# Kernel optimization log

Measured on AMD Instinct MI355X. Metric: run time of the kernel, lower is better.

Reference implementation:

```python
import jax, jax.numpy as jnp
import numpy as np

L = 3          # encoder layers
H, D = 12, 64  # heads, head_dim
DM = H * D     # 768
DF = 3072
WH = WW = 14
S = WH * WW + 1            # 197 tokens incl. cls
ND = (2*WH-1)*(2*WW-1) + 3  # 732 rel-pos entries
EPS = 1e-12


def _make_rel_idx():
    coords = np.stack(np.meshgrid(np.arange(WH), np.arange(WW), indexing='ij'))
    coords = coords.reshape(2, -1)                      # [2, 196]
    rel = (coords[:, :, None] - coords[:, None, :]).transpose(1, 2, 0)  # [196,196,2]
    rel[:, :, 0] += WH - 1
    rel[:, :, 1] += WW - 1
    rel[:, :, 0] *= 2 * WW - 1
    idx = np.zeros((S, S), dtype=np.int32)
    idx[1:, 1:] = rel.sum(-1)
    idx[0, :] = ND - 3
    idx[:, 0] = ND - 2
    idx[0, 0] = ND - 1
    return jnp.asarray(idx.flatten())

REL_IDX = _make_rel_idx()


def _ln(x, g, b):
    m = jnp.mean(x, -1, keepdims=True)
    v = jnp.mean(jnp.square(x - m), -1, keepdims=True)
    return (x - m) * jax.lax.rsqrt(v + EPS) * g + b


def setup_inputs() -> dict:
    key = jax.random.key(0)
    ks = iter(jax.random.split(key, 32))
    p = lambda *s: jax.random.normal(next(ks), s, jnp.float32) * 0.02
    inp = {
        'x': jax.random.normal(next(ks), (64, WH, WW, DM), jnp.float32),
        'cls': p(1, 1, DM),
        'g1': jnp.ones((L, DM)), 'b1': jnp.zeros((L, DM)),
        'Wq': p(L, DM, DM), 'bq': jnp.zeros((L, DM)),
        'Wk': p(L, DM, DM),
        'Wv': p(L, DM, DM), 'bv': jnp.zeros((L, DM)),
        'rel_tbl': p(L, ND, H),
        'Wo': p(L, DM, DM), 'bo': jnp.zeros((L, DM)),
        'lam1': jnp.full((L, DM), 0.1),
        'g2': jnp.ones((L, DM)), 'b2': jnp.zeros((L, DM)),
        'Wi': p(L, DM, DF), 'bi': jnp.zeros((L, DF)),
        'Wmo': p(L, DF, DM), 'bmo': jnp.zeros((L, DM)),
        'lam2': jnp.full((L, DM), 0.1),
    }
    return inp


def reference(x, cls, g1, b1, Wq, bq, Wk, Wv, bv, rel_tbl, Wo, bo, lam1,
              g2, b2, Wi, bi, Wmo, bmo, lam2):
    B = x.shape[0]
    # patchemb: NHWC -> NCHW -> [B, C, HW] -> [B, HW, C], prepend cls token
    t = jnp.transpose(x, (0, 3, 1, 2)).reshape(B, DM, WH * WW)
    t = jnp.transpose(t, (0, 2, 1))
    h = jnp.concatenate([jnp.broadcast_to(cls, (B, 1, DM)), t], axis=1)  # [B,S,DM]

    scale = 1.0 / np.sqrt(D)
    for i in range(L):
        r = h
        hn = _ln(h, g1[i], b1[i])
        q = (hn @ Wq[i] + bq[i]).reshape(B, S, H, D)
        k = (hn @ Wk[i]).reshape(B, S, H, D)
        v = (hn @ Wv[i] + bv[i]).reshape(B, S, H, D)
        scores = jnp.einsum('bqhd,bkhd->bhqk', q, k) * scale   # [B,H,S,S]
        rel = rel_tbl[i][REL_IDX].reshape(S, S, H)             # gather bias table
        scores = scores + jnp.transpose(rel, (2, 0, 1))[None]
        probs = jax.nn.softmax(scores, axis=-1)
        ctx = jnp.einsum('bhqk,bkhd->bqhd', probs, v).reshape(B, S, DM)
        h = r + (ctx @ Wo[i] + bo[i]) * lam1[i]
        r = h
        hn = _ln(h, g2[i], b2[i])
        ff = jax.nn.gelu(hn @ Wi[i] + bi[i], approximate=False) @ Wmo[i] + bmo[i]
        h = r + ff * lam2[i]
    return h  # final encoder output [B, S, DM]
```

## Files before the change

kernel.cpp:

```cpp
#include <hip/hip_runtime.h>

#define DMM 768
#define DFF 3072
#define NH  12
#define HD  64
#define SQ  197
#define BA  64
#define NDD 732
#define MROWS (BA*SQ)
#define MPAD  12672
#define PCOLS 224
#define KS2   72
#define VTS   232
#define QS    2304

typedef unsigned short u16;
typedef __bf16 bf16x8 __attribute__((ext_vector_type(8)));
typedef float  f32x4  __attribute__((ext_vector_type(4)));
typedef unsigned short us8 __attribute__((ext_vector_type(8)));

__device__ __forceinline__ float b2f(u16 u) {
    unsigned v = ((unsigned)u) << 16;
    float f; __builtin_memcpy(&f, &v, 4); return f;
}
__device__ __forceinline__ u16 f2b(float f) {
    unsigned v; __builtin_memcpy(&v, &f, 4);
    unsigned r = v + 0x7FFFu + ((v >> 16) & 1u);
    return (u16)(r >> 16);
}
__device__ __forceinline__ float gelu_exact(float x) {
    return 0.5f * x * (1.0f + erff(x * 0.70710678118654752f));
}
__device__ __forceinline__ void gload16(const u16* g, u16* l) {
    __builtin_amdgcn_global_load_lds(
        (const __attribute__((address_space(1))) unsigned int*)(g),
        (__attribute__((address_space(3))) unsigned int*)(l), 16, 0, 0);
}
__device__ __forceinline__ void hard_barrier() {
    asm volatile("s_waitcnt lgkmcnt(0)" ::: "memory");
    __builtin_amdgcn_s_barrier();
}

__global__ void patch_k(const float* __restrict__ x, const float* __restrict__ cls,
                        float* __restrict__ h) {
    long idx = (long)blockIdx.x * 256 + threadIdx.x;
    if (idx >= (long)MPAD * DMM) return;
    long r = idx / DMM; int c = (int)(idx % DMM);
    float v = 0.0f;
    if (r < MROWS) {
        int b = (int)(r / SQ), s = (int)(r % SQ);
        v = (s == 0) ? cls[c] : x[((long)b * 196 + (s - 1)) * DMM + c];
    }
    h[idx] = v;
}

__global__ void out_k(const float* __restrict__ h, float* __restrict__ out) {
    long idx = (long)blockIdx.x * 256 + threadIdx.x;
    if (idx < (long)MROWS * DMM) out[idx] = h[idx];
}

__global__ __launch_bounds__(256) void tcast_k(const float* __restrict__ in,
                                               u16* __restrict__ out,
                                               int Kd, int Nd) {
    __shared__ float t[32][33];
    int k0 = blockIdx.x * 32, n0 = blockIdx.y * 32;
    int tx = threadIdx.x & 31, ty = threadIdx.x >> 5;
    #pragma unroll
    for (int i = 0; i < 4; ++i)
        t[tx][ty + 8 * i] = in[(long)(k0 + ty + 8 * i) * Nd + n0 + tx];
    __syncthreads();
    #pragma unroll
    for (int i = 0; i < 4; ++i)
        out[(long)(n0 + ty + 8 * i) * Kd + k0 + tx] = f2b(t[ty + 8 * i][tx]);
}

__global__ __launch_bounds__(256) void ln_k(const float* __restrict__ h,
                                            const float* __restrict__ g,
                                            const float* __restrict__ b,
                                            u16* __restrict__ hn) {
    int row = blockIdx.x, tid = threadIdx.x;
    const float* hr = h + (long)row * DMM;
    float x0 = hr[tid], x1 = hr[tid + 256], x2 = hr[tid + 512];
    float s = x0 + x1 + x2, sq = x0 * x0 + x1 * x1 + x2 * x2;
    #pragma unroll
    for (int m = 32; m > 0; m >>= 1) {
        s  += __shfl_xor(s,  m, 64);
        sq += __shfl_xor(sq, m, 64);
    }
    __shared__ float ls[4], lq[4];
    int w = tid >> 6;
    if ((tid & 63) == 0) { ls[w] = s; lq[w] = sq; }
    __syncthreads();
    s  = ls[0] + ls[1] + ls[2] + ls[3];
    sq = lq[0] + lq[1] + lq[2] + lq[3];
    float mean = s * (1.0f / DMM);
    float var  = fmaxf(sq * (1.0f / DMM) - mean * mean, 0.0f);
    float rs = rsqrtf(var + 1e-12f);
    u16* hnr = hn + (long)row * DMM;
    hnr[tid]       = f2b((x0 - mean) * rs * g[tid]       + b[tid]);
    hnr[tid + 256] = f2b((x1 - mean) * rs * g[tid + 256] + b[tid + 256]);
    hnr[tid + 512] = f2b((x2 - mean) * rs * g[tid + 512] + b[tid + 512]);
}

__global__ void bqkv_k(const float* __restrict__ bq, const float* __restrict__ bv,
                       float* __restrict__ out) {
    int i = blockIdx.x * 256 + threadIdx.x;
    if (i >= QS) return;
    out[i] = (i < 768) ? bq[i] : ((i < 1536) ? 0.0f : bv[i - 1536]);
}

template <int EPI>
__global__ __launch_bounds__(256) void gemm_bt(
    const u16* __restrict__ A, const u16* __restrict__ BT,
    const float* __restrict__ bias, u16* __restrict__ outB,
    float* __restrict__ hio, const float* __restrict__ lam,
    int K, int N) {
    __shared__ __align__(16) u16 pool[16896];
    int tid = threadIdx.x;
    int w = tid >> 6, lane = tid & 63;
    int wr = w >> 1, wc = w & 1;
    int m16 = lane & 15;
    int kq  = (lane >> 4) * 8;
    int kq4 = (lane >> 4) * 4;

    int nwg = gridDim.x, bid = blockIdx.x;
    int qd = nwg >> 3, rm = nwg & 7;
    int xcd = bid & 7, seq = bid >> 3;
    int wg = (xcd < rm ? xcd * (qd + 1) : rm * (qd + 1) + (xcd - rm) * qd) + seq;
    int ntn = N >> 7;
    long m0 = (long)(wg / ntn) * 128;
    long n0 = (long)(wg % ntn) * 128;

    f32x4 acc[4][4] = {};

    int row_a = tid >> 2;
    int col_a = (tid & 3) * 8;
    const u16* gA0 = &A[(m0 + row_a) * (long)K + col_a];
    const u16* gA1 = &A[(m0 + 64 + row_a) * (long)K + col_a];
    const u16* gB0 = &BT[(n0 + row_a) * (long)K + col_a];
    const u16* gB1 = &BT[(n0 + 64 + row_a) * (long)K + col_a];
    int wo = w * 512;

    u16* const b0 = pool;
    u16* const b1 = pool + 8192;

    auto stage = [&](int k, u16* buf) {
        int k0 = k << 5;
        gload16(gA0 + k0, buf + wo);
        gload16(gA1 + k0, buf + 2048 + wo);
        gload16(gB0 + k0, buf + 4096 + wo);
        gload16(gB1 + k0, buf + 6144 + wo);
    };
    auto compute = [&](const u16* buf) {
        bf16x8 af[4], bf[4];
        #pragma unroll
        for (int i = 0; i < 4; ++i)
            af[i] = *(const bf16x8*)&buf[(wr * 64 + i * 16 + m16) * 32 + kq];
        #pragma unroll
        for (int j = 0; j < 4; ++j)
            bf[j] = *(const bf16x8*)&buf[4096 + (wc * 64 + j * 16 + m16) * 32 + kq];
        #pragma unroll
        for (int i = 0; i < 4; ++i)
            #pragma unroll
            for (int j = 0; j < 4; ++j)
                acc[i][j] = __builtin_amdgcn_mfma_f32_16x16x32_bf16(
                    af[i], bf[j], acc[i][j], 0, 0, 0);
    };

    const int nsteps = K >> 5;
    stage(0, b0);
    for (int ks = 0; ks < nsteps - 2; ks += 2) {
        stage(ks + 1, b1);
        asm volatile("s_waitcnt vmcnt(4)" ::: "memory");
        __builtin_amdgcn_s_barrier();
        compute(b0);
        hard_barrier();
        stage(ks + 2, b0);
        asm volatile("s_waitcnt vmcnt(4)" ::: "memory");
        __builtin_amdgcn_s_barrier();
        compute(b1);
        hard_barrier();
    }
    stage(nsteps - 1, b1);
    asm volatile("s_waitcnt vmcnt(4)" ::: "memory");
    __builtin_amdgcn_s_barrier();
    compute(b0);
    hard_barrier();
    asm volatile("s_waitcnt vmcnt(0)" ::: "memory");
    __builtin_amdgcn_s_barrier();
    compute(b1);

    hard_barrier();
    float* Cs = (float*)pool;
    float bcol[4];
    #pragma unroll
    for (int j = 0; j < 4; ++j)
        bcol[j] = bias ? bias[n0 + wc * 64 + j * 16 + m16] : 0.0f;
    int et4 = tid * 4;
    int colr = et4 & 127;
    f32x4 lam4 = {};
    if (EPI == 2) lam4 = *(const f32x4*)&lam[n0 + colr];

    #pragma unroll
    for (int p = 0; p < 2; ++p) {
        if (p) hard_barrier();
        if (wr == p) {
            #pragma unroll
            for (int i = 0; i < 4; ++i)
                #pragma unroll
                for (int j = 0; j < 4; ++j)
                    #pragma unroll
                    for (int r = 0; r < 4; ++r)
                        Cs[(i * 16 + kq4 + r) * 132 + wc * 64 + j * 16 + m16] =
                            acc[i][j][r] + bcol[j];
        }
        hard_barrier();
        #pragma unroll
        for (int k = 0; k < 8; ++k) {
            int e0 = k * 1024 + et4;
            int row = e0 >> 7;
            f32x4 v = *(const f32x4*)&Cs[row * 132 + colr];
            long gi = (m0 + p * 64 + row) * (long)N + n0 + colr;
            if (EPI == 0) {
                uint2 o;
                o.x = (unsigned)f2b(v[0]) | ((unsigned)f2b(v[1]) << 16);
                o.y = (unsigned)f2b(v[2]) | ((unsigned)f2b(v[3]) << 16);
                *(uint2*)&outB[gi] = o;
            } else if (EPI == 1) {
                uint2 o;
                o.x = (unsigned)f2b(gelu_exact(v[0])) | ((unsigned)f2b(gelu_exact(v[1])) << 16);
                o.y = (unsigned)f2b(gelu_exact(v[2])) | ((unsigned)f2b(gelu_exact(v[3])) << 16);
                *(uint2*)&outB[gi] = o;
            } else {
                f32x4 hv = *(f32x4*)&hio[gi];
                #pragma unroll
                for (int t = 0; t < 4; ++t) hv[t] += v[t] * lam4[t];
                *(f32x4*)&hio[gi] = hv;
            }
        }
    }
}

__device__ __forceinline__ int relidx(int q, int k) {
    if (q == 0 && k == 0) return NDD - 1;
    if (k == 0) return NDD - 2;
    if (q == 0) return NDD - 3;
    int a = q - 1, c = k - 1;
    int dh = a / 14 - c / 14 + 13;
    int dw = a % 14 - c % 14 + 13;
    return dh * 27 + dw;
}

__global__ void bias_k(const float* __restrict__ rel, float* __restrict__ bias) {
    int idx = blockIdx.x * 256 + threadIdx.x;
    if (idx >= NH * 208 * 208) return;
    int hh = idx / (208 * 208);
    int r = (idx / 208) % 208, c = idx % 208;
    float v = 0.0f;
    if (r < SQ && c < SQ) v = rel[relidx(r, c) * NH + hh];
    bias[idx] = v;
}

__global__ __launch_bounds__(256) void attn_qk(
    const u16* __restrict__ QKV, const float* __restrict__ bias,
    u16* __restrict__ P) {
    int bh = blockIdx.x;
    int b = bh / NH, hh = bh % NH;
    __shared__ u16 Ks[208 * KS2];
    int tid = threadIdx.x, w = tid >> 6, lane = tid & 63;
    long base = ((long)b * SQ) * QS + hh * HD;
    const u16* Qp = QKV;
    const u16* Kp = QKV + 768;
    u16* Pb = P + (long)bh * 208 * PCOLS;
    for (int idx = tid; idx < 208 * 16; idx += 256)
        Pb[(idx >> 4) * PCOLS + 208 + (idx & 15)] = 0;
    for (int idx = tid; idx < 208 * 8; idx += 256) {
        int row = idx >> 3, dg = (idx & 7) * 8;
        us8 kv = {};
        if (row < SQ) kv = *(const us8*)&Kp[base + (long)row * QS + dg];
        *(us8*)&Ks[row * KS2 + dg] = kv;
    }
    __syncthreads();
    int m16 = lane & 15, quad = lane >> 4;
    int kq8 = quad * 8, q4 = quad * 4;
    const float* bh_bias = bias + (long)hh * 208 * 208;
    for (int t = w; t < 13; t += 4) {
        int m0 = t * 16;
        int qrow = m0 + m16; if (qrow > SQ - 1) qrow = SQ - 1;
        bf16x8 a0 = *(const bf16x8*)&Qp[base + (long)qrow * QS + kq8];
        bf16x8 a1 = *(const bf16x8*)&Qp[base + (long)qrow * QS + 32 + kq8];
        f32x4 sc[13];
        #pragma unroll
        for (int n = 0; n < 13; ++n) {
            bf16x8 b0 = *(const bf16x8*)&Ks[(n * 16 + m16) * KS2 + kq8];
            bf16x8 b1 = *(const bf16x8*)&Ks[(n * 16 + m16) * KS2 + 32 + kq8];
            f32x4 z = {};
            z = __builtin_amdgcn_mfma_f32_16x16x32_bf16(a0, b0, z, 0, 0, 0);
            z = __builtin_amdgcn_mfma_f32_16x16x32_bf16(a1, b1, z, 0, 0, 0);
            sc[n] = z;
        }
        float mx[4] = {-3e38f, -3e38f, -3e38f, -3e38f};
        #pragma unroll
        for (int n = 0; n < 13; ++n) {
            int col = n * 16 + m16;
            bool valid = col < SQ;
            #pragma unroll
            for (int r = 0; r < 4; ++r) {
                float v = sc[n][r] * 0.125f + bh_bias[(m0 + q4 + r) * 208 + col];
                v = valid ? v : -3e38f;
                sc[n][r] = v;
                mx[r] = fmaxf(mx[r], v);
            }
        }
        #pragma unroll
        for (int r = 0; r < 4; ++r)
            #pragma unroll
            for (int msk = 1; msk < 16; msk <<= 1)
                mx[r] = fmaxf(mx[r], __shfl_xor(mx[r], msk, 64));
        float sum[4] = {0, 0, 0, 0};
        #pragma unroll
        for (int n = 0; n < 13; ++n)
            #pragma unroll
            for (int r = 0; r < 4; ++r) {
                float e = __expf(sc[n][r] - mx[r]);
                sc[n][r] = e;
                sum[r] += e;
            }
        #pragma unroll
        for (int r = 0; r < 4; ++r)
            #pragma unroll
            for (int msk = 1; msk < 16; msk <<= 1)
                sum[r] += __shfl_xor(sum[r], msk, 64);
        float inv[4];
        #pragma unroll
        for (int r = 0; r < 4; ++r) inv[r] = 1.0f / sum[r];
        #pragma unroll
        for (int n = 0; n < 13; ++n) {
            int col = n * 16 + m16;
            #pragma unroll
            for (int r = 0; r < 4; ++r)
                Pb[(m0 + q4 + r) * PCOLS + col] = f2b(sc[n][r] * inv[r]);
        }
    }
}

__global__ __launch_bounds__(256) void attn_pv(
    const u16* __restrict__ P, const u16* __restrict__ QKV,
    u16* __restrict__ ctx) {
    int bh = blockIdx.x;
    int b = bh / NH, hh = bh % NH;
    __shared__ u16 Vt[64 * VTS];
    int tid = threadIdx.x, w = tid >> 6, lane = tid & 63;
    long base  = ((long)b * SQ) * QS + 1536 + hh * HD;
    long basec = ((long)b * SQ) * DMM + hh * HD;
    const u16* Vp = QKV;
    for (int idx = tid; idx < 224 * 8; idx += 256) {
        int row = idx >> 3, dg = (idx & 7) * 8;
        us8 vv = {};
        if (row < SQ) vv = *(const us8*)&Vp[base + (long)row * QS + dg];
        #pragma unroll
        for (int j = 0; j < 8; ++j) Vt[(dg + j) * VTS + row] = vv[j];
    }
    __syncthreads();
    const u16* Pb = P + (long)bh * 208 * PCOLS;
    int m16 = lane & 15, quad = lane >> 4;
    int kq8 = quad * 8, q4 = quad * 4;
    for (int t = w; t < 13; t += 4) {
        int m0 = t * 16;
        f32x4 co[4] = {};
        #pragma unroll
        for (int ks = 0; ks < 7; ++ks) {
            bf16x8 ap = *(const bf16x8*)&Pb[(m0 + m16) * PCOLS + ks * 32 + kq8];
            #pragma unroll
            for (int n = 0; n < 4; ++n) {
                bf16x8 bv = *(const bf16x8*)&Vt[(n * 16 + m16) * VTS + ks * 32 + kq8];
                co[n] = __builtin_amdgcn_mfma_f32_16x16x32_bf16(ap, bv, co[n], 0, 0, 0);
            }
        }
        #pragma unroll
        for (int n = 0; n < 4; ++n) {
            int col = n * 16 + m16;
            #pragma unroll
            for (int r = 0; r < 4; ++r) {
                int qr = m0 + q4 + r;
                if (qr < SQ) ctx[basec + (long)qr * DMM + col] = f2b(co[n][r]);
            }
        }
    }
}

extern "C" void kernel_launch(void* const* d_in, const int* in_sizes, int n_in,
                              void* d_out, int out_size, void* d_ws, size_t ws_size,
                              hipStream_t stream) {
    const float* x    = (const float*)d_in[0];
    const float* cls  = (const float*)d_in[1];
    const float* g1   = (const float*)d_in[2];
    const float* b1   = (const float*)d_in[3];
    const float* Wq   = (const float*)d_in[4];
    const float* bq   = (const float*)d_in[5];
    const float* Wk   = (const float*)d_in[6];
    const float* Wv   = (const float*)d_in[7];
    const float* bv   = (const float*)d_in[8];
    const float* rel  = (const float*)d_in[9];
    const float* Wo   = (const float*)d_in[10];
    const float* bo   = (const float*)d_in[11];
    const float* lam1 = (const float*)d_in[12];
    const float* g2   = (const float*)d_in[13];
    const float* b2   = (const float*)d_in[14];
    const float* Wi   = (const float*)d_in[15];
    const float* bi   = (const float*)d_in[16];
    const float* Wmo  = (const float*)d_in[17];
    const float* bmo  = (const float*)d_in[18];
    const float* lam2 = (const float*)d_in[19];

    char* p = (char*)d_ws;
    auto alloc = [&](size_t bytes) -> void* {
        void* r = (void*)p;
        p += (bytes + 255) & ~(size_t)255;
        return r;
    };
    float* h     = (float*)alloc((size_t)MPAD * DMM * 4);
    u16*   hn    = (u16*)alloc((size_t)MPAD * DMM * 2);
    u16*   qkvb  = (u16*)alloc((size_t)MPAD * QS * 2);
    u16*   ffh   = (u16*)alloc((size_t)MPAD * DFF * 2);
    u16*   WqkvT = (u16*)alloc((size_t)QS * DMM * 2);
    u16*   WoT   = (u16*)alloc((size_t)DMM * DMM * 2);
    u16*   WiT   = (u16*)alloc((size_t)DMM * DFF * 2);
    u16*   WmoT  = (u16*)alloc((size_t)DFF * DMM * 2);
    float* biasb = (float*)alloc((size_t)NH * 208 * 208 * 4);
    float* bqkv  = (float*)alloc((size_t)QS * 4);
    u16*   ctxb  = hn;
    u16*   Pbuf  = ffh;

    patch_k<<<((long)MPAD * DMM + 255) / 256, 256, 0, stream>>>(x, cls, h);

    dim3 tg1(DMM / 32, DMM / 32);
    dim3 tg2(DMM / 32, DFF / 32);
    dim3 tg3(DFF / 32, DMM / 32);
    int gqkv = (MPAD / 128) * (QS / 128);
    int g6   = (MPAD / 128) * (DMM / 128);
    int g24  = (MPAD / 128) * (DFF / 128);

    for (int i = 0; i < 3; ++i) {
        size_t wofs  = (size_t)i * DMM * DMM;
        size_t wofs2 = (size_t)i * DMM * DFF;
        tcast_k<<<tg1, 256, 0, stream>>>(Wq + wofs, WqkvT,                 DMM, DMM);
        tcast_k<<<tg1, 256, 0, stream>>>(Wk + wofs, WqkvT + 768 * DMM,     DMM, DMM);
        tcast_k<<<tg1, 256, 0, stream>>>(Wv + wofs, WqkvT + 2 * 768 * DMM, DMM, DMM);
        tcast_k<<<tg1, 256, 0, stream>>>(Wo + wofs, WoT, DMM, DMM);
        tcast_k<<<tg2, 256, 0, stream>>>(Wi + wofs2, WiT, DMM, DFF);
        tcast_k<<<tg3, 256, 0, stream>>>(Wmo + wofs2, WmoT, DFF, DMM);
        bias_k<<<(NH * 208 * 208 + 255) / 256, 256, 0, stream>>>(rel + (size_t)i * NDD * NH, biasb);
        bqkv_k<<<(QS + 255) / 256, 256, 0, stream>>>(bq + i * DMM, bv + i * DMM, bqkv);

        ln_k<<<MPAD, 256, 0, stream>>>(h, g1 + i * DMM, b1 + i * DMM, hn);
        gemm_bt<0><<<gqkv, 256, 0, stream>>>(hn, WqkvT, bqkv, qkvb, nullptr, nullptr, DMM, QS);
        attn_qk<<<BA * NH, 256, 0, stream>>>(qkvb, biasb, Pbuf);
        attn_pv<<<BA * NH, 256, 0, stream>>>(Pbuf, qkvb, ctxb);
        gemm_bt<2><<<g6, 256, 0, stream>>>(ctxb, WoT, bo + i * DMM, nullptr, h, lam1 + i * DMM, DMM, DMM);
        ln_k<<<MPAD, 256, 0, stream>>>(h, g2 + i * DMM, b2 + i * DMM, hn);
        gemm_bt<1><<<g24, 256, 0, stream>>>(hn, WiT, bi + i * DFF, ffh, nullptr, nullptr, DMM, DFF);
        gemm_bt<2><<<g6, 256, 0, stream>>>(ffh, WmoT, bmo + i * DMM, nullptr, h, lam2 + i * DMM, DFF, DMM);
    }

    out_k<<<((long)MROWS * DMM + 255) / 256, 256, 0, stream>>>(h, (float*)d_out);
}
```

Baseline: 1.383 ms.

## Triple-buffer GEMM k-loop with MFMA priority; fuse weight-cast and bias launches

The GEMM main loop moves from double to triple LDS buffering. Each k-step now issues the next tile's loads right after the barrier, and the trailing hard barrier per step is dropped. MFMA blocks are wrapped in s_setprio to favour math issue. Separately, the four 768x768 weight transposes are merged into one launch using grid z, and the bqkv bias fill is folded into bias_k, cutting launch count. The cost is larger LDS use per GEMM block (about 48KB), which may lower occupancy. With fewer barriers there is also some risk of LDS read/write overlap between waves.

```diff
diff --git a/kernel.cpp b/kernel.cpp
--- a/kernel.cpp
+++ b/kernel.cpp
@@ -13,6 +13,7 @@
 #define KS2   72
 #define VTS   232
 #define QS    2304
+#define BIASN (NH*208*208)
 
 typedef unsigned short u16;
 typedef __bf16 bf16x8 __attribute__((ext_vector_type(8)));
@@ -72,6 +73,26 @@
     #pragma unroll
     for (int i = 0; i < 4; ++i)
         out[(long)(n0 + ty + 8 * i) * Kd + k0 + tx] = f2b(t[ty + 8 * i][tx]);
+}
+
+__global__ __launch_bounds__(256) void tcast4_k(
+    const float* __restrict__ s0, const float* __restrict__ s1,
+    const float* __restrict__ s2, const float* __restrict__ s3,
+    u16* __restrict__ d0, u16* __restrict__ d1,
+    u16* __restrict__ d2, u16* __restrict__ d3) {
+    __shared__ float t[32][33];
+    int z = blockIdx.z;
+    const float* in = (z == 0) ? s0 : (z == 1) ? s1 : (z == 2) ? s2 : s3;
+    u16* out = (z == 0) ? d0 : (z == 1) ? d1 : (z == 2) ? d2 : d3;
+    int k0 = blockIdx.x * 32, n0 = blockIdx.y * 32;
+    int tx = threadIdx.x & 31, ty = threadIdx.x >> 5;
+    #pragma unroll
+    for (int i = 0; i < 4; ++i)
+        t[tx][ty + 8 * i] = in[(long)(k0 + ty + 8 * i) * DMM + n0 + tx];
+    __syncthreads();
+    #pragma unroll
+    for (int i = 0; i < 4; ++i)
+        out[(long)(n0 + ty + 8 * i) * DMM + k0 + tx] = f2b(t[ty + 8 * i][tx]);
 }
 
 __global__ __launch_bounds__(256) void ln_k(const float* __restrict__ h,
@@ -102,20 +123,13 @@
     hnr[tid + 512] = f2b((x2 - mean) * rs * g[tid + 512] + b[tid + 512]);
 }
 
-__global__ void bqkv_k(const float* __restrict__ bq, const float* __restrict__ bv,
-                       float* __restrict__ out) {
-    int i = blockIdx.x * 256 + threadIdx.x;
-    if (i >= QS) return;
-    out[i] = (i < 768) ? bq[i] : ((i < 1536) ? 0.0f : bv[i - 1536]);
-}
-
 template <int EPI>
 __global__ __launch_bounds__(256) void gemm_bt(
     const u16* __restrict__ A, const u16* __restrict__ BT,
     const float* __restrict__ bias, u16* __restrict__ outB,
     float* __restrict__ hio, const float* __restrict__ lam,
     int K, int N) {
-    __shared__ __align__(16) u16 pool[16896];
+    __shared__ __align__(16) u16 pool[24576];
     int tid = threadIdx.x;
     int w = tid >> 6, lane = tid & 63;
     int wr = w >> 1, wc = w & 1;
@@ -143,6 +157,7 @@
 
     u16* const b0 = pool;
     u16* const b1 = pool + 8192;
+    u16* const b2 = pool + 16384;
 
     auto stage = [&](int k, u16* buf) {
         int k0 = k << 5;
@@ -159,36 +174,45 @@
         #pragma unroll
         for (int j = 0; j < 4; ++j)
             bf[j] = *(const bf16x8*)&buf[4096 + (wc * 64 + j * 16 + m16) * 32 + kq];
+        __builtin_amdgcn_s_setprio(1);
         #pragma unroll
         for (int i = 0; i < 4; ++i)
             #pragma unroll
             for (int j = 0; j < 4; ++j)
                 acc[i][j] = __builtin_amdgcn_mfma_f32_16x16x32_bf16(
                     af[i], bf[j], acc[i][j], 0, 0, 0);
+        __builtin_amdgcn_s_setprio(0);
     };
 
     const int nsteps = K >> 5;
     stage(0, b0);
-    for (int ks = 0; ks < nsteps - 2; ks += 2) {
-        stage(ks + 1, b1);
+    stage(1, b1);
+    const int niter = nsteps / 3 - 1;
+    for (int it = 0; it < niter; ++it) {
+        int k = it * 3;
         asm volatile("s_waitcnt vmcnt(4)" ::: "memory");
         __builtin_amdgcn_s_barrier();
+        stage(k + 2, b2);
         compute(b0);
-        hard_barrier();
-        stage(ks + 2, b0);
         asm volatile("s_waitcnt vmcnt(4)" ::: "memory");
         __builtin_amdgcn_s_barrier();
+        stage(k + 3, b0);
         compute(b1);
-        hard_barrier();
-    }
-    stage(nsteps - 1, b1);
+        asm volatile("s_waitcnt vmcnt(4)" ::: "memory");
+        __builtin_amdgcn_s_barrier();
+        stage(k + 4, b1);
+        compute(b2);
+    }
     asm volatile("s_waitcnt vmcnt(4)" ::: "memory");
     __builtin_amdgcn_s_barrier();
+    stage(nsteps - 1, b2);
     compute(b0);
-    hard_barrier();
+    asm volatile("s_waitcnt vmcnt(4)" ::: "memory");
+    __builtin_amdgcn_s_barrier();
+    compute(b1);
     asm volatile("s_waitcnt vmcnt(0)" ::: "memory");
     __builtin_amdgcn_s_barrier();
-    compute(b1);
+    compute(b2);
 
     hard_barrier();
     float* Cs = (float*)pool;
@@ -251,14 +275,21 @@
     return dh * 27 + dw;
 }
 
-__global__ void bias_k(const float* __restrict__ rel, float* __restrict__ bias) {
+__global__ void bias_k(const float* __restrict__ rel, float* __restrict__ bias,
+                       const float* __restrict__ bq, const float* __restrict__ bv,
+                       float* __restrict__ bqkv) {
     int idx = blockIdx.x * 256 + threadIdx.x;
-    if (idx >= NH * 208 * 208) return;
-    int hh = idx / (208 * 208);
-    int r = (idx / 208) % 208, c = idx % 208;
-    float v = 0.0f;
-    if (r < SQ && c < SQ) v = rel[relidx(r, c) * NH + hh];
-    bias[idx] = v;
+    if (idx < BIASN) {
+        int hh = idx / (208 * 208);
+        int r = (idx / 208) % 208, c = idx % 208;
+        float v = 0.0f;
+        if (r < SQ && c < SQ) v = rel[relidx(r, c) * NH + hh];
+        bias[idx] = v;
+    } else {
+        int i = idx - BIASN;
+        if (i < QS)
+            bqkv[i] = (i < 768) ? bq[i] : ((i < 1536) ? 0.0f : bv[i - 1536]);
+    }
 }
 
 __global__ __launch_bounds__(256) void attn_qk(
@@ -434,7 +465,7 @@
 
     patch_k<<<((long)MPAD * DMM + 255) / 256, 256, 0, stream>>>(x, cls, h);
 
-    dim3 tg1(DMM / 32, DMM / 32);
+    dim3 tg4(DMM / 32, DMM / 32, 4);
     dim3 tg2(DMM / 32, DFF / 32);
     dim3 tg3(DFF / 32, DMM / 32);
     int gqkv = (MPAD / 128) * (QS / 128);
@@ -444,14 +475,13 @@
     for (int i = 0; i < 3; ++i) {
         size_t wofs  = (size_t)i * DMM * DMM;
         size_t wofs2 = (size_t)i * DMM * DFF;
-        tcast_k<<<tg1, 256, 0, stream>>>(Wq + wofs, WqkvT,                 DMM, DMM);
-        tcast_k<<<tg1, 256, 0, stream>>>(Wk + wofs, WqkvT + 768 * DMM,     DMM, DMM);
-        tcast_k<<<tg1, 256, 0, stream>>>(Wv + wofs, WqkvT + 2 * 768 * DMM, DMM, DMM);
-        tcast_k<<<tg1, 256, 0, stream>>>(Wo + wofs, WoT, DMM, DMM);
+        tcast4_k<<<tg4, 256, 0, stream>>>(Wq + wofs, Wk + wofs, Wv + wofs, Wo + wofs,
+                                          WqkvT, WqkvT + 768 * DMM,
+                                          WqkvT + 2 * 768 * DMM, WoT);
         tcast_k<<<tg2, 256, 0, stream>>>(Wi + wofs2, WiT, DMM, DFF);
         tcast_k<<<tg3, 256, 0, stream>>>(Wmo + wofs2, WmoT, DFF, DMM);
-        bias_k<<<(NH * 208 * 208 + 255) / 256, 256, 0, stream>>>(rel + (size_t)i * NDD * NH, biasb);
-        bqkv_k<<<(QS + 255) / 256, 256, 0, stream>>>(bq + i * DMM, bv + i * DMM, bqkv);
+        bias_k<<<(BIASN + QS + 255) / 256, 256, 0, stream>>>(
+            rel + (size_t)i * NDD * NH, biasb, bq + i * DMM, bv + i * DMM, bqkv);
 
         ln_k<<<MPAD, 256, 0, stream>>>(h, g1 + i * DMM, b1 + i * DMM, hn);
         gemm_bt<0><<<gqkv, 256, 0, stream>>>(hn, WqkvT, bqkv, qkvb, nullptr, nullptr, DMM, QS);
```

Result: no change. 1.378 ms (-0.4%).
